# Kernel tuning notes

Hardware: AMD Instinct MI355X
Metric: run time of the kernel (lower is better)

## Reference

```python
import jax, jax.numpy as jnp
import numpy as np

B, N, F, P, E, T = 8, 10000, 8, 12, 160000, 64
C = 32  # A3TGCN2 out_channels fixed to 32 in the module


def setup_inputs() -> dict:
    key = jax.random.key(0)
    ks = jax.random.split(key, 20)
    x = jax.random.normal(ks[0], (B, N, F, P), jnp.float32)
    edge_index = jax.random.randint(ks[1], (2, E), 0, N, dtype=jnp.int64)
    edge_weight = jax.random.uniform(ks[2], (E,), jnp.float32)

    def g(k, shape):
        return jax.random.normal(k, shape, jnp.float32) * 0.05

    return dict(
        x=x, edge_index=edge_index, edge_weight=edge_weight,
        Wz=g(ks[3], (F, C)), bz=g(ks[4], (C,)),
        Wr=g(ks[5], (F, C)), br=g(ks[6], (C,)),
        Wh=g(ks[7], (F, C)), bh=g(ks[8], (C,)),
        Lz_w=g(ks[9], (2 * C, C)), Lz_b=g(ks[10], (C,)),
        Lr_w=g(ks[11], (2 * C, C)), Lr_b=g(ks[12], (C,)),
        Lh_w=g(ks[13], (2 * C, C)), Lh_b=g(ks[14], (C,)),
        att=g(ks[15], (P,)),
        lin1_w=g(ks[16], (C, P)), lin1_b=g(ks[17], (P,)),
        lin2_w=g(ks[18], (N, T)), lin2_b=g(ks[19], (T,)),
    )


def _gcn_norm(edge_index, edge_weight, n):
    # GCNConv default: add self-loops (weight 1) + symmetric normalization
    row, col = edge_index[0], edge_index[1]
    loop = jnp.arange(n)
    row = jnp.concatenate([row, loop])
    col = jnp.concatenate([col, loop])
    w = jnp.concatenate([edge_weight, jnp.ones((n,), edge_weight.dtype)])
    deg = jax.ops.segment_sum(w, col, num_segments=n)
    dis = jnp.where(deg > 0, jax.lax.rsqrt(jnp.where(deg > 0, deg, 1.0)), 0.0)
    return row, col, dis[row] * w * dis[col]


def _gcn_conv(X, W, b, row, col, norm, n):
    XW = X @ W                                   # [B,N,C]
    msg = XW[:, row, :] * norm[None, :, None]    # gather over source nodes
    out = jnp.zeros((X.shape[0], n, W.shape[1]), X.dtype).at[:, col, :].add(msg)
    return out + b


def reference(x, edge_index, edge_weight, Wz, bz, Wr, br, Wh, bh,
              Lz_w, Lz_b, Lr_w, Lr_b, Lh_w, Lh_b, att,
              lin1_w, lin1_b, lin2_w, lin2_b):
    b_, n, _, periods = x.shape
    row, col, norm = _gcn_norm(edge_index, edge_weight, n)
    probs = jax.nn.softmax(att)
    # A3TGCN2 passes H=None to the TGCN cell at every period -> hidden state
    # is zeros for every period (faithful to library implementation).
    H0 = jnp.zeros((b_, n, Lz_w.shape[1]), x.dtype)
    H_accum = jnp.zeros_like(H0)
    for p in range(periods):
        Xp = x[:, :, :, p]                       # [B,N,F]
        Z = jax.nn.sigmoid(
            jnp.concatenate([_gcn_conv(Xp, Wz, bz, row, col, norm, n), H0], axis=2) @ Lz_w + Lz_b)
        R = jax.nn.sigmoid(
            jnp.concatenate([_gcn_conv(Xp, Wr, br, row, col, norm, n), H0], axis=2) @ Lr_w + Lr_b)
        Ht = jnp.tanh(
            jnp.concatenate([_gcn_conv(Xp, Wh, bh, row, col, norm, n), H0 * R], axis=2) @ Lh_w + Lh_b)
        H = Z * H0 + (1.0 - Z) * Ht
        H_accum = H_accum + probs[p] * H
    h = jax.nn.relu(H_accum)                     # [B,N,32]
    h = h @ lin1_w + lin1_b                      # [B,N,P]
    h = jnp.swapaxes(h, 2, 1)                    # [B,P,N]
    h = h @ lin2_w + lin2_b                      # [B,P,T]
    return jnp.swapaxes(h, 2, 1)                 # [B,T,P]
```

## Files before the change

kernel.cpp:

```cpp
#include <hip/hip_runtime.h>
#include <stdint.h>

#define NN 10000
#define NNP 10016
#define NB 8
#define NP 12
#define NT 64
#define NC 32
#define BCAP 64
#define FCN 80
#define FCH 125
#define XB 3750

typedef float v2f __attribute__((ext_vector_type(2)));

__device__ __forceinline__ v2f up2(unsigned u) {
    v2f r;
    r.x = __uint_as_float(u << 16);
    r.y = __uint_as_float(u & 0xffff0000u);
    return r;
}
__device__ __forceinline__ v2f sp(float v) { v2f r; r.x = v; r.y = v; return r; }

__global__ __launch_bounds__(1024) void k_zero(int* __restrict__ p) {
    p[blockIdx.x * 1024 + threadIdx.x] = 0;
}

__global__ __launch_bounds__(256) void k_prep(
    const float* __restrict__ x,
    const int* __restrict__ rowp, const int* __restrict__ colp, const float* __restrict__ ew,
    const float* __restrict__ Wz, const float* __restrict__ bz,
    const float* __restrict__ Wh, const float* __restrict__ bh,
    const float* __restrict__ Lzw, const float* __restrict__ Lzb,
    const float* __restrict__ Lhw, const float* __restrict__ Lhb,
    const float* __restrict__ att,
    float* __restrict__ sm, float* __restrict__ deg, int* __restrict__ count,
    uint2* __restrict__ bucket, unsigned short* __restrict__ xh,
    int E, int EB) {
    const int blk = blockIdx.x, tid = threadIdx.x;
    if (blk < XB) {
        const int s = blk * 256 + tid;
        const int b = s / 120000, rem = s - b * 120000;
        const int n = rem / 12, q = rem - n * 12;
        const float* px = x + (size_t)b * 960000 + n * 96 + q * 8;
        const float4 f0 = *(const float4*)px;
        const float4 f1 = *(const float4*)(px + 4);
        unsigned u0, u1, u2, u3;
        asm("v_cvt_pk_bf16_f32 %0, %1, %2" : "=v"(u0) : "v"(f0.x), "v"(f0.y));
        asm("v_cvt_pk_bf16_f32 %0, %1, %2" : "=v"(u1) : "v"(f0.z), "v"(f0.w));
        asm("v_cvt_pk_bf16_f32 %0, %1, %2" : "=v"(u2) : "v"(f1.x), "v"(f1.y));
        asm("v_cvt_pk_bf16_f32 %0, %1, %2" : "=v"(u3) : "v"(f1.z), "v"(f1.w));
        *(uint4*)(xh + ((size_t)(b * NNP + n) * 12 + q) * 8) = make_uint4(u0, u1, u2, u3);
    } else if (blk < XB + EB) {
        const int e = (blk - XB) * 256 + tid;
        if (e < E) {
            const int c = colp[e];
            const float w = ew[e];
            atomicAdd(&deg[c], w);
            const int slot = atomicAdd(&count[c], 1);
            if (slot < BCAP) bucket[slot * NN + c] = make_uint2((unsigned)rowp[e], __float_as_uint(w));
        }
    } else {
        const int t = tid, f = t >> 5, c = t & 31;
        float mz = 0.f, mh = 0.f;
        for (int j = 0; j < NC; ++j) {
            mz += Wz[f * NC + j] * Lzw[j * NC + c];
            mh += Wh[f * NC + j] * Lhw[j * NC + c];
        }
        sm[16 + 2 * t]     = mz;
        sm[16 + 2 * t + 1] = mh;
        if (t < NC) {
            float cz = Lzb[t], ch = Lhb[t];
            for (int j = 0; j < NC; ++j) {
                cz += bz[j] * Lzw[j * NC + t];
                ch += bh[j] * Lhw[j * NC + t];
            }
            sm[528 + 2 * t]     = cz;
            sm[528 + 2 * t + 1] = ch;
        }
        if (t == 0) {
            float m = -1e30f;
            for (int p = 0; p < NP; ++p) m = fmaxf(m, att[p]);
            float e[NP]; float s = 0.f;
            for (int p = 0; p < NP; ++p) { e[p] = __expf(att[p] - m); s += e[p]; }
            for (int p = 0; p < NP; ++p) sm[p] = e[p] / s;
        }
    }
}

__global__ __launch_bounds__(256) void k_main(
    const unsigned short* __restrict__ xh, const float* __restrict__ deg,
    const int* __restrict__ count, const uint2* __restrict__ bucket,
    const float* __restrict__ sm,
    const float* __restrict__ l1w, const float* __restrict__ l1b,
    float* __restrict__ h1t) {
    __shared__ float sY[4][800];
    __shared__ float sHA[4][264];
    __shared__ uint2 sE[4][64];

    const int tid = threadIdx.x;
    const int wv = tid >> 6, l = tid & 63;
    const int b = blockIdx.x & 7;
    const int chunk = blockIdx.x >> 3;
    const int g = l >> 3, j8 = l & 7;
    const int n = chunk * 32 + wv * 8 + g;
    const char* xb = (const char*)(xh + (size_t)b * NNP * 96);

    const int cnt = min(count[n], BCAP);
    const float dn = rsqrtf(deg[n] + 1.0f);
    v2f A[6];
    {
        const v2f vsn = sp(dn * dn);
        const char* p0 = xb + ((unsigned)n * 192u + (unsigned)j8 * 24u);
        const uint2 u0 = *(const uint2*)p0;
        const uint2 u1 = *(const uint2*)(p0 + 8);
        const uint2 u2 = *(const uint2*)(p0 + 16);
        A[0] = up2(u0.x) * vsn; A[1] = up2(u0.y) * vsn;
        A[2] = up2(u1.x) * vsn; A[3] = up2(u1.y) * vsn;
        A[4] = up2(u2.x) * vsn; A[5] = up2(u2.y) * vsn;
    }

    int mcnt = cnt;
    #pragma unroll
    for (int off = 1; off < 64; off <<= 1) mcnt = max(mcnt, __shfl_xor(mcnt, off));

    uint2* sEw = &sE[wv][0];
    for (int base = 0; base < mcnt; base += 8) {
        uint2 ent = make_uint2(0u, 0u);
        const int e = base + j8;
        if (e < cnt) {
            const uint2 be = bucket[e * NN + n];
            const float nrm = rsqrtf(deg[be.x] + 1.0f) * __uint_as_float(be.y) * dn;
            ent = make_uint2(be.x * 192u, __float_as_uint(nrm));
        }
        sEw[l] = ent;
        #pragma unroll
        for (int j = 0; j < 8; ++j) {
            const uint2 e2 = sEw[g * 8 + j];
            const v2f w = sp(__uint_as_float(e2.y));
            const char* p = xb + (e2.x + (unsigned)j8 * 24u);
            const uint2 u0 = *(const uint2*)p;
            const uint2 u1 = *(const uint2*)(p + 8);
            const uint2 u2 = *(const uint2*)(p + 16);
            A[0] = __builtin_elementwise_fma(up2(u0.x), w, A[0]);
            A[1] = __builtin_elementwise_fma(up2(u0.y), w, A[1]);
            A[2] = __builtin_elementwise_fma(up2(u1.x), w, A[2]);
            A[3] = __builtin_elementwise_fma(up2(u1.y), w, A[3]);
            A[4] = __builtin_elementwise_fma(up2(u2.x), w, A[4]);
            A[5] = __builtin_elementwise_fma(up2(u2.y), w, A[5]);
        }
    }
    {
        float* yp = &sY[wv][g * 100 + j8 * 12];
        *(float4*)yp       = make_float4(A[0].x, A[0].y, A[1].x, A[1].y);
        *(float4*)(yp + 4) = make_float4(A[2].x, A[2].y, A[3].x, A[3].y);
        *(float4*)(yp + 8) = make_float4(A[4].x, A[4].y, A[5].x, A[5].y);
    }

    const int c = l & 31;
    const float2* __restrict__ smzh = (const float2*)(sm + 16);
    const float2* __restrict__ sczh = (const float2*)(sm + 528);
    v2f m8[8];
    #pragma unroll
    for (int f = 0; f < 8; ++f) { const float2 t2 = smzh[f * 32 + c]; v2f v; v.x = t2.x; v.y = t2.y; m8[f] = v; }
    v2f czh;
    { const float2 t2 = sczh[c]; czh.x = t2.x; czh.y = t2.y; }
    float pr[12];
    #pragma unroll
    for (int p = 0; p < 12; ++p) pr[p] = sm[p];

    #pragma unroll
    for (int t4 = 0; t4 < 4; ++t4) {
        const int nd = t4 * 2 + (l >> 5);
        const float* yb = &sY[wv][nd * 100];
        v2f zh[12];
        #pragma unroll
        for (int p = 0; p < 12; ++p) zh[p] = czh;
        #pragma unroll
        for (int f = 0; f < 8; ++f) {
            const float4 y0 = *(const float4*)(yb + f * 12);
            const float4 y1 = *(const float4*)(yb + f * 12 + 4);
            const float4 y2 = *(const float4*)(yb + f * 12 + 8);
            const v2f mm = m8[f];
            zh[0]  = __builtin_elementwise_fma(sp(y0.x), mm, zh[0]);
            zh[1]  = __builtin_elementwise_fma(sp(y0.y), mm, zh[1]);
            zh[2]  = __builtin_elementwise_fma(sp(y0.z), mm, zh[2]);
            zh[3]  = __builtin_elementwise_fma(sp(y0.w), mm, zh[3]);
            zh[4]  = __builtin_elementwise_fma(sp(y1.x), mm, zh[4]);
            zh[5]  = __builtin_elementwise_fma(sp(y1.y), mm, zh[5]);
            zh[6]  = __builtin_elementwise_fma(sp(y1.z), mm, zh[6]);
            zh[7]  = __builtin_elementwise_fma(sp(y1.w), mm, zh[7]);
            zh[8]  = __builtin_elementwise_fma(sp(y2.x), mm, zh[8]);
            zh[9]  = __builtin_elementwise_fma(sp(y2.y), mm, zh[9]);
            zh[10] = __builtin_elementwise_fma(sp(y2.z), mm, zh[10]);
            zh[11] = __builtin_elementwise_fma(sp(y2.w), mm, zh[11]);
        }
        float hacc = 0.f;
        #pragma unroll
        for (int p = 0; p < 12; ++p) {
            const float u = __expf(-zh[p].x);
            const float v = __expf(2.f * zh[p].y);
            const float num = u * (v - 1.f);
            const float den = fmaf(u, v, u) + (v + 1.f);
            hacc = fmaf(pr[p] * num, __builtin_amdgcn_rcpf(den), hacc);
        }
        sHA[wv][nd * 33 + c] = fmaxf(hacc, 0.f);
    }

    const int n0w = chunk * 32 + wv * 8;
    {
        const int nd = l / 12, p = l - nd * 12;
        if (nd < 8) {
            float s = l1b[p];
            #pragma unroll
            for (int cc = 0; cc < 32; ++cc) s = fmaf(sHA[wv][nd * 33 + cc], l1w[cc * 12 + p], s);
            const int nn = n0w + nd;
            if (nn < NN) h1t[nn * 96 + b * 12 + p] = s;
        }
    }
    if (l < 32) {
        const int task = l + 64;
        const int nd = task / 12, p = task - nd * 12;
        float s = l1b[p];
        #pragma unroll
        for (int cc = 0; cc < 32; ++cc) s = fmaf(sHA[wv][nd * 33 + cc], l1w[cc * 12 + p], s);
        const int nn = n0w + nd;
        if (nn < NN) h1t[nn * 96 + b * 12 + p] = s;
    }
}

__global__ __launch_bounds__(256) void k_final(const float* __restrict__ h1t, const float* __restrict__ W2,
                                               float* __restrict__ partial) {
    __shared__ float sh1[96 * FCN];
    const int tid = threadIdx.x;
    const int n0 = blockIdx.x * FCN;

    for (int idx = tid; idx < 96 * FCN; idx += 256) {
        const int nn = idx / 96, i = idx - nn * 96;
        sh1[i * FCN + nn] = h1t[(n0 + nn) * 96 + i];
    }
    __syncthreads();

    const int t = tid & 63, w = tid >> 6;
    const float* sh = &sh1[w * 24 * FCN];
    float acc[24];
    #pragma unroll
    for (int j = 0; j < 24; ++j) acc[j] = 0.f;

    for (int nn = 0; nn < FCN; nn += 4) {
        const float w20 = W2[(n0 + nn + 0) * NT + t];
        const float w21 = W2[(n0 + nn + 1) * NT + t];
        const float w22 = W2[(n0 + nn + 2) * NT + t];
        const float w23 = W2[(n0 + nn + 3) * NT + t];
        #pragma unroll
        for (int j = 0; j < 24; ++j) {
            const float4 hv = *(const float4*)&sh[j * FCN + nn];
            acc[j] = fmaf(hv.x, w20, fmaf(hv.y, w21, fmaf(hv.z, w22, fmaf(hv.w, w23, acc[j]))));
        }
    }

    float* pp = partial + blockIdx.x * 6144 + w * 24 * 64 + t;
    #pragma unroll
    for (int j = 0; j < 24; ++j) pp[j * 64] = acc[j];
}

__global__ __launch_bounds__(256) void k_red(const float* __restrict__ partial, const float* __restrict__ l2b,
                                             float* __restrict__ out) {
    __shared__ float red[4][64];
    const int i = blockIdx.x;
    const int t = threadIdx.x & 63, g = threadIdx.x >> 6;
    float s = 0.f;
    for (int c = g; c < FCH; c += 4)
        s += partial[c * 6144 + i * 64 + t];
    red[g][t] = s;
    __syncthreads();
    if (g == 0) {
        const float v = red[0][t] + red[1][t] + red[2][t] + red[3][t] + l2b[t];
        const int b = i / 12, p = i - b * 12;
        out[b * 768 + t * 12 + p] = v;
    }
}

extern "C" void kernel_launch(void* const* d_in, const int* in_sizes, int n_in,
                              void* d_out, int out_size, void* d_ws, size_t ws_size,
                              hipStream_t stream) {
    const float* x    = (const float*)d_in[0];
    const int*   eidx = (const int*)d_in[1];
    const float* ew   = (const float*)d_in[2];
    const float* Wz   = (const float*)d_in[3];
    const float* bz   = (const float*)d_in[4];
    const float* Wh   = (const float*)d_in[7];
    const float* bh   = (const float*)d_in[8];
    const float* Lzw  = (const float*)d_in[9];
    const float* Lzb  = (const float*)d_in[10];
    const float* Lhw  = (const float*)d_in[13];
    const float* Lhb  = (const float*)d_in[14];
    const float* att  = (const float*)d_in[15];
    const float* l1w  = (const float*)d_in[16];
    const float* l1b  = (const float*)d_in[17];
    const float* W2   = (const float*)d_in[18];
    const float* l2b  = (const float*)d_in[19];
    float* out = (float*)d_out;
    const int E = in_sizes[2];
    const int EB = (E + 255) / 256;

    float* deg    = (float*)d_ws;
    int*   count  = (int*)(deg + 10240);
    uint2* bucket = (uint2*)(count + 10240);
    float* sm     = (float*)(bucket + NN * BCAP);
    float* h1t    = sm + 1024;
    unsigned short* xh = (unsigned short*)(h1t + NN * 96);
    float* partial = (float*)(xh + (size_t)NB * NNP * 96);

    const int* rowp = eidx;
    const int* colp = eidx + E;

    hipLaunchKernelGGL(k_zero, dim3(20), dim3(1024), 0, stream, (int*)d_ws);
    hipLaunchKernelGGL(k_prep, dim3(XB + EB + 1), dim3(256), 0, stream,
                       x, rowp, colp, ew, Wz, bz, Wh, bh, Lzw, Lzb, Lhw, Lhb, att,
                       sm, deg, count, bucket, xh, E, EB);
    hipLaunchKernelGGL(k_main, dim3(313 * 8), dim3(256), 0, stream,
                       xh, deg, count, bucket, sm, l1w, l1b, h1t);
    hipLaunchKernelGGL(k_final, dim3(FCH), dim3(256), 0, stream, h1t, W2, partial);
    hipLaunchKernelGGL(k_red, dim3(96), dim3(256), 0, stream, partial, l2b, out);
}
```

Baseline: 112.4 us.

## Sort nodes by in-degree bucket to balance wave work in main kernel

Adds a single-block counting-sort kernel that orders nodes by edge count, in descending order, and precomputes the inverse-sqrt degrees. The main kernel then processes nodes in that permuted order, so the 8 nodes within a wave have similar edge counts and the wave-wide max loop wastes fewer iterations. This removes load imbalance from divergent per-node edge counts. The cost is an extra serial single-block launch, indirection through perm, and scattered h1t writes.

After: 119.9 us. +6.6%, slower.

```diff
diff --git a/kernel.cpp b/kernel.cpp
--- a/kernel.cpp
+++ b/kernel.cpp
@@ -88,10 +88,34 @@
     }
 }
 
+__global__ __launch_bounds__(1024) void k_sort(const float* __restrict__ deg, const int* __restrict__ count,
+                                               float* __restrict__ dis, int* __restrict__ perm) {
+    __shared__ int hist[BCAP + 1];
+    __shared__ int base_[BCAP + 1];
+    const int tid = threadIdx.x;
+    if (tid <= BCAP) hist[tid] = 0;
+    __syncthreads();
+    for (int n = tid; n < NN; n += 1024) {
+        dis[n] = rsqrtf(deg[n] + 1.0f);
+        atomicAdd(&hist[min(count[n], BCAP)], 1);
+    }
+    __syncthreads();
+    if (tid == 0) {
+        int acc = 0;
+        for (int b = BCAP; b >= 0; --b) { base_[b] = acc; acc += hist[b]; }
+    }
+    __syncthreads();
+    for (int n = tid; n < NN; n += 1024) {
+        const int b = min(count[n], BCAP);
+        const int pos = atomicAdd(&base_[b], 1);
+        perm[pos] = n;
+    }
+}
+
 __global__ __launch_bounds__(256) void k_main(
-    const unsigned short* __restrict__ xh, const float* __restrict__ deg,
+    const unsigned short* __restrict__ xh, const float* __restrict__ dis,
     const int* __restrict__ count, const uint2* __restrict__ bucket,
-    const float* __restrict__ sm,
+    const int* __restrict__ perm, const float* __restrict__ sm,
     const float* __restrict__ l1w, const float* __restrict__ l1b,
     float* __restrict__ h1t) {
     __shared__ float sY[4][800];
@@ -103,11 +127,13 @@
     const int b = blockIdx.x & 7;
     const int chunk = blockIdx.x >> 3;
     const int g = l >> 3, j8 = l & 7;
-    const int n = chunk * 32 + wv * 8 + g;
+    const int sid = chunk * 32 + wv * 8 + g;
+    const bool valid = sid < NN;
+    const int n = valid ? perm[sid] : 0;
     const char* xb = (const char*)(xh + (size_t)b * NNP * 96);
 
-    const int cnt = min(count[n], BCAP);
-    const float dn = rsqrtf(deg[n] + 1.0f);
+    const int cnt = valid ? min(count[n], BCAP) : 0;
+    const float dn = dis[n];
     v2f A[6];
     {
         const v2f vsn = sp(dn * dn);
@@ -130,7 +156,7 @@
         const int e = base + j8;
         if (e < cnt) {
             const uint2 be = bucket[e * NN + n];
-            const float nrm = rsqrtf(deg[be.x] + 1.0f) * __uint_as_float(be.y) * dn;
+            const float nrm = dis[be.x] * __uint_as_float(be.y) * dn;
             ent = make_uint2(be.x * 192u, __float_as_uint(nrm));
         }
         sEw[l] = ent;
@@ -207,25 +233,31 @@
         sHA[wv][nd * 33 + c] = fmaxf(hacc, 0.f);
     }
 
-    const int n0w = chunk * 32 + wv * 8;
+    const int s0w = chunk * 32 + wv * 8;
     {
         const int nd = l / 12, p = l - nd * 12;
         if (nd < 8) {
+            const int sidn = s0w + nd;
+            if (sidn < NN) {
+                const int nn = perm[sidn];
+                float s = l1b[p];
+                #pragma unroll
+                for (int cc = 0; cc < 32; ++cc) s = fmaf(sHA[wv][nd * 33 + cc], l1w[cc * 12 + p], s);
+                h1t[nn * 96 + b * 12 + p] = s;
+            }
+        }
+    }
+    if (l < 32) {
+        const int task = l + 64;
+        const int nd = task / 12, p = task - nd * 12;
+        const int sidn = s0w + nd;
+        if (sidn < NN) {
+            const int nn = perm[sidn];
             float s = l1b[p];
             #pragma unroll
             for (int cc = 0; cc < 32; ++cc) s = fmaf(sHA[wv][nd * 33 + cc], l1w[cc * 12 + p], s);
-            const int nn = n0w + nd;
-            if (nn < NN) h1t[nn * 96 + b * 12 + p] = s;
-        }
-    }
-    if (l < 32) {
-        const int task = l + 64;
-        const int nd = task / 12, p = task - nd * 12;
-        float s = l1b[p];
-        #pragma unroll
-        for (int cc = 0; cc < 32; ++cc) s = fmaf(sHA[wv][nd * 33 + cc], l1w[cc * 12 + p], s);
-        const int nn = n0w + nd;
-        if (nn < NN) h1t[nn * 96 + b * 12 + p] = s;
+            h1t[nn * 96 + b * 12 + p] = s;
+        }
     }
 }
 
@@ -306,7 +338,9 @@
 
     float* deg    = (float*)d_ws;
     int*   count  = (int*)(deg + 10240);
-    uint2* bucket = (uint2*)(count + 10240);
+    float* dis    = (float*)(count + 10240);
+    int*   perm   = (int*)(dis + 10240);
+    uint2* bucket = (uint2*)(perm + 10240);
     float* sm     = (float*)(bucket + NN * BCAP);
     float* h1t    = sm + 1024;
     unsigned short* xh = (unsigned short*)(h1t + NN * 96);
@@ -319,8 +353,9 @@
     hipLaunchKernelGGL(k_prep, dim3(XB + EB + 1), dim3(256), 0, stream,
                        x, rowp, colp, ew, Wz, bz, Wh, bh, Lzw, Lzb, Lhw, Lhb, att,
                        sm, deg, count, bucket, xh, E, EB);
+    hipLaunchKernelGGL(k_sort, dim3(1), dim3(1024), 0, stream, deg, count, dis, perm);
     hipLaunchKernelGGL(k_main, dim3(313 * 8), dim3(256), 0, stream,
-                       xh, deg, count, bucket, sm, l1w, l1b, h1t);
+                       xh, dis, count, bucket, perm, sm, l1w, l1b, h1t);
     hipLaunchKernelGGL(k_final, dim3(FCH), dim3(256), 0, stream, h1t, W2, partial);
     hipLaunchKernelGGL(k_red, dim3(96), dim3(256), 0, stream, partial, l2b, out);
 }
```
